# Performance work log

Hardware: AMD Instinct MI355X
Metric: run time of the kernel (lower is better)

Reference implementation:

```python
import jax, jax.numpy as jnp
import numpy as np

PS = 5   # patch width (hardcoded ps=5 in Aggregation0)
C = 3    # rgb channels


def setup_inputs() -> dict:
    key = jax.random.key(0)
    images, hor_f, ver_f = 2, 14, C * PS * PS  # ver_f = 75
    H = W = 160
    nh = nw = H - PS + 1                       # 156 valid patch positions per side
    patches = nh * nw                          # 24336
    t = images * hor_f                         # 28 pseudo-frames
    K = 14
    k1, k2 = jax.random.split(key)
    x = jax.random.normal(k1, (images, patches, hor_f, ver_f), jnp.float32)
    nlDists = jax.random.uniform(k2, (t, patches, K), jnp.float32)
    # top-1 neighbor is the patch itself (LIDIA convention) -> full coverage, wx > 0
    j = jnp.arange(patches)
    hi = j // nw
    wi = j % nw
    ti = jnp.arange(t)
    self_ind = jnp.stack([
        jnp.broadcast_to(ti[:, None], (t, patches)),
        jnp.broadcast_to(hi[None, :], (t, patches)),
        jnp.broadcast_to(wi[None, :], (t, patches)),
    ], axis=-1)                                # [t, p, 3]
    nlInds = jnp.broadcast_to(self_ind[:, :, None, :], (t, patches, K, 3)).astype(jnp.int32)
    return {"x": x, "nlDists": nlDists, "nlInds": nlInds, "pixels_h": H, "pixels_w": W}


def _agg0(x, nlDists, nlInds, H, W):
    images, patches, hor_f, ver_f = x.shape
    t = images * hor_f
    N = t * patches
    # x.permute(0,2,3,1).view(t, ver_f, p) then 't (c h w) p -> (t p) c h w'
    xr = jnp.transpose(x, (0, 2, 3, 1)).reshape(t, ver_f, patches)
    pat = jnp.transpose(xr, (0, 2, 1)).reshape(N, C, PS, PS)
    # top-1 neighbor only
    w = jnp.exp(-nlDists[:, :, 0].reshape(N))          # [N]
    inds = nlInds[:, :, 0, :].reshape(N, 3)
    ti, hi, wi = inds[:, 0], inds[:, 1], inds[:, 2]
    d = jnp.arange(PS)
    # flat spatial index per patch pixel: [N, ps, ps]
    sidx = (ti[:, None, None] * (H * W)
            + (hi[:, None, None] + d[None, :, None]) * W
            + (wi[:, None, None] + d[None, None, :])).reshape(-1)
    # dnls.simple.gather: weighted scatter-add of patches into image + weight image
    vals = (w[:, None, None, None] * pat).transpose(0, 2, 3, 1).reshape(-1, C)
    img = jnp.zeros((t * H * W, C), x.dtype).at[sidx].add(vals)
    wimg = jnp.zeros((t * H * W,), x.dtype).at[sidx].add(jnp.repeat(w, PS * PS))
    img = img / wimg[:, None]                          # x = x / wx
    # dnls.simple.scatter: gather patches back out of the normalized image
    out_pat = img[sidx].reshape(N, PS, PS, C).transpose(0, 3, 1, 2)   # [N, c, ps, ps]
    out = out_pat.reshape(t, patches, ver_f)                          # scatter2fold
    # original: .view(images, hor_f, ver_f, patches).permute(0, 3, 1, 2)
    out = out.reshape(images, hor_f, ver_f, patches).transpose(0, 3, 1, 2)
    return out


def reference(x, nlDists, nlInds, pixels_h, pixels_w):
    return _agg0(x, nlDists, nlInds, pixels_h, pixels_w)
```

## Files before the change

### kernel.cpp

```cpp
#include <hip/hip_runtime.h>
#include <math.h>

#define PS      5
#define NCH     3
#define HOR_F   14
#define VER_F   75
#define HH      160
#define WW      160
#define NH      156
#define NW      156
#define PATCHES (NH*NW)
#define IMAGES  2
#define TT      (IMAGES*HOR_F)
#define KNN     14
#define REC_F   (HOR_F*VER_F)

__device__ __forceinline__ void gload_lds(const float* g, float* l) {
    __builtin_amdgcn_global_load_lds((const __attribute__((address_space(1))) void*)g,
                                     (__attribute__((address_space(3))) void*)l,
                                     4, 0, 0);
}

__global__ void k_weights(const float* __restrict__ nlDists,
                          float* __restrict__ w, int n) {
    int i = blockIdx.x * blockDim.x + threadIdx.x;
    if (i < n) w[i] = expf(-nlDists[(size_t)i * KNN]);
}

#define TX 16
#define TY 16
#define MAXR   (TY + PS - 1)
#define MAXREC (MAXR * MAXR)

__global__ __launch_bounds__(256)
void k_aggregate(const float* __restrict__ x,
                 const float* __restrict__ w,
                 float* __restrict__ img) {
    __shared__ float lds_x[MAXREC * VER_F];
    __shared__ float lds_w[MAXREC];

    const int x0 = blockIdx.x * TX;
    const int y0 = blockIdx.y * TY;
    const int ti = blockIdx.z;
    const int im = ti / HOR_F;
    const int hf = ti % HOR_F;
    const int tid = threadIdx.x;

    const int hi_lo = max(0, y0 - (PS - 1));
    const int hi_hi = min(NH - 1, y0 + TY - 1);
    const int wi_lo = max(0, x0 - (PS - 1));
    const int wi_hi = min(NW - 1, x0 + TX - 1);
    const int nrh = hi_hi - hi_lo + 1;
    const int nrw = wi_hi - wi_lo + 1;

    for (int rh = 0; rh < nrh; ++rh) {
        const int p_row = (hi_lo + rh) * NW + wi_lo;
        const float* gx = x + ((size_t)(im * PATCHES + p_row) * HOR_F + hf) * VER_F;
        float* ldst = lds_x + rh * nrw * VER_F;
        const int tot = nrw * VER_F;
        for (int k = tid; k < tot; k += 256) {
            int rw = k / VER_F;
            int e  = k - rw * VER_F;
            gload_lds(gx + (size_t)rw * REC_F + e, ldst + k);
        }
        if (tid < nrw)
            gload_lds(w + (size_t)ti * PATCHES + p_row + tid, lds_w + rh * nrw + tid);
    }
    __syncthreads();

    const int txl = tid % TX, tyl = tid / TX;
    const int xp = x0 + txl, yp = y0 + tyl;

    float sw = 0.f, s0 = 0.f, s1 = 0.f, s2 = 0.f;
    #pragma unroll
    for (int dy = 0; dy < PS; ++dy) {
        int hi = yp - dy;
        bool vy = (hi >= 0) & (hi < NH);
        int rh = hi - hi_lo;
        #pragma unroll
        for (int dx = 0; dx < PS; ++dx) {
            int wi = xp - dx;
            bool v = vy & (wi >= 0) & (wi < NW);
            int rec = rh * nrw + (wi - wi_lo);
            rec = v ? rec : 0;
            float wv = v ? lds_w[rec] : 0.f;
            const float* lb = lds_x + rec * VER_F + dy * PS + dx;
            sw += wv;
            s0 += wv * lb[0];
            s1 += wv * lb[25];
            s2 += wv * lb[50];
        }
    }
    float inv = 1.0f / sw;
    size_t o = ((size_t)(ti * HH + yp) * WW + xp) * NCH;
    img[o]     = s0 * inv;
    img[o + 1] = s1 * inv;
    img[o + 2] = s2 * inv;
}

#define TM 64
#define TP 64

__global__ __launch_bounds__(256)
void k_out(const float* __restrict__ img, float* __restrict__ out) {
    __shared__ float tile[TM][TP + 1];

    const int p2_0 = blockIdx.x * TP;
    const int m0   = blockIdx.y * TM;
    const int im   = blockIdx.z;
    const int tid  = threadIdx.x;
    const int lane = tid & 63;
    const int grp  = tid >> 6;

    #pragma unroll
    for (int r = 0; r < 16; ++r) {
        int ml = r * 4 + grp;
        int m  = m0 + ml;
        int p2 = p2_0 + lane;
        if (m < REC_F && p2 < PATCHES) {
            int hf  = m / VER_F;
            int vf2 = m - VER_F * hf;
            int L0  = vf2 * PATCHES + p2_0;
            int p0  = L0 / VER_F;
            int r0  = L0 - VER_F * p0;
            int j     = r0 + lane;
            int carry = (j >= VER_F) ? 1 : 0;
            int vf    = j - (carry ? VER_F : 0);
            int hi0 = p0 / NW;
            int wi0 = p0 - NW * hi0;
            int wi  = wi0 + carry;
            int hi  = hi0;
            if (wi >= NW) { wi = 0; hi += 1; }
            int c  = vf / 25;
            int r2 = vf - 25 * c;
            int dy = r2 / 5;
            int dx = r2 - 5 * dy;
            int y  = hi + dy;
            int xx = wi + dx;
            tile[ml][lane] =
                img[(((size_t)((im * HOR_F + hf) * HH + y)) * WW + xx) * NCH + c];
        }
    }
    __syncthreads();

    #pragma unroll
    for (int r = 0; r < 16; ++r) {
        int p2l = r * 4 + grp;
        int p2  = p2_0 + p2l;
        int m   = m0 + lane;
        if (p2 < PATCHES && m < REC_F) {
            out[(size_t)(im * PATCHES + p2) * REC_F + m] = tile[lane][p2l];
        }
    }
}

extern "C" void kernel_launch(void* const* d_in, const int* in_sizes, int n_in,
                              void* d_out, int out_size, void* d_ws, size_t ws_size,
                              hipStream_t stream) {
    const float* x       = (const float*)d_in[0];
    const float* nlDists = (const float*)d_in[1];
    float* out = (float*)d_out;

    float* w   = (float*)d_ws;
    float* img = w + (size_t)TT * PATCHES;

    const int NP = TT * PATCHES;

    k_weights<<<(NP + 255) / 256, 256, 0, stream>>>(nlDists, w, NP);
    k_aggregate<<<dim3(WW / TX, HH / TY, TT), 256, 0, stream>>>(x, w, img);
    k_out<<<dim3((PATCHES + TP - 1) / TP, (REC_F + TM - 1) / TM, IMAGES),
            256, 0, stream>>>(img, out);
}
```

Before: 520.1 us.

## Split aggregate halo load into two phases, swizzle tile order, vectorize output stores

The aggregate kernel now loads the patch halo in two row phases with a smaller LDS buffer, which cuts the shared-memory footprint roughly in half so more blocks fit per CU. The cost is an extra barrier and a second serialized load. The grid becomes 1D with a tile permutation that interleaves blocks across groups of the tile space. The output transpose kernel writes float2 pairs instead of scalars; this relies on REC_F being even and on 8-byte alignment.

```diff
diff --git a/kernel.cpp b/kernel.cpp
--- a/kernel.cpp
+++ b/kernel.cpp
@@ -15,7 +15,7 @@
 #define KNN     14
 #define REC_F   (HOR_F*VER_F)
 
-__device__ __forceinline__ void gload_lds(const float* g, float* l) {
+__device__ __forceinline__ void gload_lds4(const float* g, float* l) {
     __builtin_amdgcn_global_load_lds((const __attribute__((address_space(1))) void*)g,
                                      (__attribute__((address_space(3))) void*)l,
                                      4, 0, 0);
@@ -29,19 +29,23 @@
 
 #define TX 16
 #define TY 16
-#define MAXR   (TY + PS - 1)
-#define MAXREC (MAXR * MAXR)
+#define MAXRW   (TX + PS - 1)
+#define PH_ROWS 10
+#define NTILES  ((WW/TX) * (HH/TY) * TT)
 
 __global__ __launch_bounds__(256)
 void k_aggregate(const float* __restrict__ x,
                  const float* __restrict__ w,
                  float* __restrict__ img) {
-    __shared__ float lds_x[MAXREC * VER_F];
-    __shared__ float lds_w[MAXREC];
+    __shared__ float lds_x[PH_ROWS * MAXRW * VER_F];
+    __shared__ float lds_w[PH_ROWS * MAXRW];
 
-    const int x0 = blockIdx.x * TX;
-    const int y0 = blockIdx.y * TY;
-    const int ti = blockIdx.z;
+    int bid  = blockIdx.x;
+    int tile = (bid & 7) * (NTILES / 8) + (bid >> 3);
+    int txy  = tile % ((WW/TX)*(HH/TY));
+    int ti   = tile / ((WW/TX)*(HH/TY));
+    const int x0 = (txy % (WW/TX)) * TX;
+    const int y0 = (txy / (WW/TX)) * TY;
     const int im = ti / HOR_F;
     const int hf = ti % HOR_F;
     const int tid = threadIdx.x;
@@ -52,45 +56,56 @@
     const int wi_hi = min(NW - 1, x0 + TX - 1);
     const int nrh = hi_hi - hi_lo + 1;
     const int nrw = wi_hi - wi_lo + 1;
-
-    for (int rh = 0; rh < nrh; ++rh) {
-        const int p_row = (hi_lo + rh) * NW + wi_lo;
-        const float* gx = x + ((size_t)(im * PATCHES + p_row) * HOR_F + hf) * VER_F;
-        float* ldst = lds_x + rh * nrw * VER_F;
-        const int tot = nrw * VER_F;
-        for (int k = tid; k < tot; k += 256) {
-            int rw = k / VER_F;
-            int e  = k - rw * VER_F;
-            gload_lds(gx + (size_t)rw * REC_F + e, ldst + k);
-        }
-        if (tid < nrw)
-            gload_lds(w + (size_t)ti * PATCHES + p_row + tid, lds_w + rh * nrw + tid);
-    }
-    __syncthreads();
+    const int NR1 = (nrh + 1) >> 1;
 
     const int txl = tid % TX, tyl = tid / TX;
     const int xp = x0 + txl, yp = y0 + tyl;
 
     float sw = 0.f, s0 = 0.f, s1 = 0.f, s2 = 0.f;
-    #pragma unroll
-    for (int dy = 0; dy < PS; ++dy) {
-        int hi = yp - dy;
-        bool vy = (hi >= 0) & (hi < NH);
-        int rh = hi - hi_lo;
+
+    for (int ph = 0; ph < 2; ++ph) {
+        const int lo = ph ? NR1 : 0;
+        const int hi = ph ? nrh : NR1;
+        if (ph) __syncthreads();
+
+        for (int rh = lo; rh < hi; ++rh) {
+            const int p_row = (hi_lo + rh) * NW + wi_lo;
+            const float* gx = x + ((size_t)(im * PATCHES + p_row) * HOR_F + hf) * VER_F;
+            float* ldst = lds_x + (rh - lo) * nrw * VER_F;
+            const int tot = nrw * VER_F;
+            for (int k = tid; k < tot; k += 256) {
+                int rw = k / VER_F;
+                int e  = k - rw * VER_F;
+                gload_lds4(gx + (size_t)rw * REC_F + e, ldst + k);
+            }
+            if (tid < nrw)
+                gload_lds4(w + (size_t)ti * PATCHES + p_row + tid,
+                           lds_w + (rh - lo) * nrw + tid);
+        }
+        __syncthreads();
+
         #pragma unroll
-        for (int dx = 0; dx < PS; ++dx) {
-            int wi = xp - dx;
-            bool v = vy & (wi >= 0) & (wi < NW);
-            int rec = rh * nrw + (wi - wi_lo);
-            rec = v ? rec : 0;
-            float wv = v ? lds_w[rec] : 0.f;
-            const float* lb = lds_x + rec * VER_F + dy * PS + dx;
-            sw += wv;
-            s0 += wv * lb[0];
-            s1 += wv * lb[25];
-            s2 += wv * lb[50];
+        for (int dy = 0; dy < PS; ++dy) {
+            int hrow = yp - dy;
+            int rh = hrow - hi_lo;
+            if (rh >= lo && rh < hi) {
+                int rbase = (rh - lo) * nrw;
+                #pragma unroll
+                for (int dx = 0; dx < PS; ++dx) {
+                    int wi = xp - dx;
+                    bool v = (wi >= 0) & (wi < NW);
+                    int rec = rbase + (v ? (wi - wi_lo) : 0);
+                    float wv = v ? lds_w[rec] : 0.f;
+                    const float* lb = lds_x + rec * VER_F + dy * PS + dx;
+                    sw += wv;
+                    s0 += wv * lb[0];
+                    s1 += wv * lb[25];
+                    s2 += wv * lb[50];
+                }
+            }
         }
     }
+
     float inv = 1.0f / sw;
     size_t o = ((size_t)(ti * HH + yp) * WW + xp) * NCH;
     img[o]     = s0 * inv;
@@ -143,13 +158,16 @@
     }
     __syncthreads();
 
+    const int mh = tid & 31;
+    const int pr = tid >> 5;
     #pragma unroll
-    for (int r = 0; r < 16; ++r) {
-        int p2l = r * 4 + grp;
+    for (int r = 0; r < 8; ++r) {
+        int p2l = r * 8 + pr;
         int p2  = p2_0 + p2l;
-        int m   = m0 + lane;
-        if (p2 < PATCHES && m < REC_F) {
-            out[(size_t)(im * PATCHES + p2) * REC_F + m] = tile[lane][p2l];
+        int m   = m0 + mh * 2;
+        if (p2 < PATCHES && m + 1 < REC_F) {
+            float2 v = make_float2(tile[mh * 2][p2l], tile[mh * 2 + 1][p2l]);
+            *reinterpret_cast<float2*>(&out[(size_t)(im * PATCHES + p2) * REC_F + m]) = v;
         }
     }
 }
@@ -167,7 +185,7 @@
     const int NP = TT * PATCHES;
 
     k_weights<<<(NP + 255) / 256, 256, 0, stream>>>(nlDists, w, NP);
-    k_aggregate<<<dim3(WW / TX, HH / TY, TT), 256, 0, stream>>>(x, w, img);
+    k_aggregate<<<NTILES, 256, 0, stream>>>(x, w, img);
     k_out<<<dim3((PATCHES + TP - 1) / TP, (REC_F + TM - 1) / TM, IMAGES),
             256, 0, stream>>>(img, out);
 }
```

Result: no change. 510.4 us (-1.9%).
